# Kernel tuning notes

Hardware: AMD Instinct MI355X
Metric: run time of the kernel (lower is better)

The kernel has to match this reference:

```python
import jax, jax.numpy as jnp
import numpy as np

B, L, D, H = 2, 1024, 1024, 16
HEAD = D // H
BUCKETS = 256
MAX_REL = 512
ATT_SPAN = BUCKETS          # pos_ebd_size = position_buckets when buckets > 0
SCALE_FACTOR = 3            # 1 (content) + 1 (c2p) + 1 (p2c)


def _log_bucket(rel, bucket_size, max_position):
    """make_log_bucket_position: signed log-bucketed relative positions."""
    sign = jnp.sign(rel).astype(jnp.float32)
    mid = bucket_size // 2
    abs_pos = jnp.where((rel < mid) & (rel > -mid), mid - 1, jnp.abs(rel)).astype(jnp.float32)
    log_pos = jnp.ceil(jnp.log(abs_pos / mid) / np.float32(np.log((max_position - 1) / mid)) * (mid - 1)) + mid
    bucket = jnp.where(abs_pos <= mid, rel.astype(jnp.float32), log_pos * sign)
    return bucket.astype(jnp.int32)


def build_relative_position(q_len, k_len):
    rel = jnp.arange(q_len, dtype=jnp.int32)[:, None] - jnp.arange(k_len, dtype=jnp.int32)[None, :]
    return _log_bucket(rel, BUCKETS, MAX_REL)  # [q_len, k_len]


def setup_inputs() -> dict:
    key = jax.random.key(0)
    ks = jax.random.split(key, 6)
    w = 0.02  # typical init scale, keeps softmax well-conditioned
    return {
        "hidden_states": jax.random.normal(ks[0], (B, L, D), jnp.float32),
        "attention_mask": jnp.ones((B, L), jnp.int32),
        "rel_embeddings": jax.random.normal(ks[1], (2 * ATT_SPAN, D), jnp.float32) * w,
        "Wq": jax.random.normal(ks[2], (D, D), jnp.float32) * w,
        "bq": jnp.zeros((D,), jnp.float32),
        "Wk": jax.random.normal(ks[3], (D, D), jnp.float32) * w,
        "bk": jnp.zeros((D,), jnp.float32),
        "Wv": jax.random.normal(ks[4], (D, D), jnp.float32) * w,
        "bv": jnp.zeros((D,), jnp.float32),
    }


def reference(hidden_states, attention_mask, rel_embeddings, Wq, bq, Wk, bk, Wv, bv):
    Bn, Ln, Dn = hidden_states.shape

    def proj(x, W, b):  # Linear with bias, torch convention y = x W^T + b
        return x @ W.T + b

    def to_heads(x):  # [.., L, D] -> [.., H, L, HEAD]
        return x.reshape(*x.shape[:-1], H, HEAD).swapaxes(-3, -2)

    q = to_heads(proj(hidden_states, Wq, bq))  # [B,H,L,d]
    k = to_heads(proj(hidden_states, Wk, bk))
    v = to_heads(proj(hidden_states, Wv, bv))

    scale = jnp.sqrt(jnp.float32(HEAD * SCALE_FACTOR))
    scores = jnp.einsum('bhqd,bhkd->bhqk', q, k) / scale

    # disentangled relative-position bias (share_att_key=True -> reuse Wq/Wk)
    rel = build_relative_position(Ln, Ln)                     # [L,L] log-bucketed
    pos_k = proj(rel_embeddings, Wk, bk).reshape(2 * ATT_SPAN, H, HEAD)
    pos_q = proj(rel_embeddings, Wq, bq).reshape(2 * ATT_SPAN, H, HEAD)

    # c2p: Q . posK, gathered at (rel + span)
    c2p_att = jnp.einsum('bhqd,phd->bhqp', q, pos_k)          # [B,H,L,2S]
    c2p_idx = jnp.clip(rel + ATT_SPAN, 0, 2 * ATT_SPAN - 1)   # [L,L]
    c2p = jnp.take_along_axis(c2p_att, jnp.broadcast_to(c2p_idx[None, None], (Bn, H, Ln, Ln)), axis=-1)

    # p2c: K . posQ gathered at (-rel + span), then transposed to [q,k]
    p2c_att = jnp.einsum('bhkd,phd->bhkp', k, pos_q)          # [B,H,L,2S]
    p2c_idx = jnp.clip(-rel + ATT_SPAN, 0, 2 * ATT_SPAN - 1)
    p2c = jnp.take_along_axis(p2c_att, jnp.broadcast_to(p2c_idx[None, None], (Bn, H, Ln, Ln)), axis=-1)
    p2c = jnp.swapaxes(p2c, -1, -2)

    scores = scores + (c2p + p2c) / scale

    bias = jnp.where(attention_mask[:, None, None, :] > 0, 0.0, -1e9).astype(scores.dtype)
    probs = jax.nn.softmax(scores + bias, axis=-1)
    ctx = jnp.einsum('bhqk,bhkd->bhqd', probs, v)
    return ctx.swapaxes(1, 2).reshape(Bn, Ln, Dn)
```

## Files before the change

### kernel.cpp

```cpp
#include <hip/hip_runtime.h>


typedef short s8v __attribute__((ext_vector_type(8)));
typedef short s4v __attribute__((ext_vector_type(4)));
typedef float f32x4 __attribute__((ext_vector_type(4)));
typedef float f4v __attribute__((ext_vector_type(4)));

#define QK_SCALE 0.26864243f

__device__ __forceinline__ unsigned short f2bf(float f) {
  unsigned u = __builtin_bit_cast(unsigned, f);
  u += 0x7fffu + ((u >> 16) & 1u);
  return (unsigned short)(u >> 16);
}
__device__ __forceinline__ float bf2f(unsigned short h) {
  unsigned u = ((unsigned)h) << 16;
  return __builtin_bit_cast(float, u);
}

__device__ __forceinline__ void gload_lds16(const void* g, void* l) {
  __builtin_amdgcn_global_load_lds(
      (const __attribute__((address_space(1))) void*)g,
      (__attribute__((address_space(3))) void*)l, 16, 0, 0);
}

__global__ __launch_bounds__(256) void prep_kernel(
    const float* __restrict__ hidden, const float* __restrict__ rel,
    const float* __restrict__ Wq, const float* __restrict__ Wk,
    const float* __restrict__ Wv, const int* __restrict__ mask,
    short* __restrict__ Abf, short* __restrict__ Wbf,
    float* __restrict__ mbias, short* __restrict__ Tt) {
  int idx = blockIdx.x * 256 + threadIdx.x;
  const int NCONV = 1441792;
  if (idx < NCONV) {
    const float* src; short* dst; int off;
    if (idx < 524288) { src = hidden; dst = Abf; off = idx; }
    else if (idx < 655360) { src = rel; dst = Abf + 2048 * 1024; off = idx - 524288; }
    else {
      int j = idx - 655360;
      int w = j / 262144; off = j - w * 262144;
      src = (w == 0) ? Wq : (w == 1) ? Wk : Wv;
      dst = Wbf + w * 1048576;
    }
    f4v v = ((const f4v*)src)[off];
    s4v o;
    o[0] = (short)f2bf(v[0]); o[1] = (short)f2bf(v[1]);
    o[2] = (short)f2bf(v[2]); o[3] = (short)f2bf(v[3]);
    ((s4v*)dst)[off] = o;
  } else {
    int j = idx - NCONV;
    if (j < 2047) {
      int r = j - 1023;
      float fr = (float)r;
      float sign = (r > 0) ? 1.f : ((r < 0) ? -1.f : 0.f);
      float abs_pos = (r < 128 && r > -128) ? 127.f : fabsf(fr);
      const float logc = 1.3843393245589053f;
      float log_pos = ceilf(logf(abs_pos * (1.f / 128.f)) / logc * 127.f) + 128.f;
      float bucket = (abs_pos <= 128.f) ? fr : log_pos * sign;
      int bi = (int)bucket + 256;
      bi = bi < 0 ? 0 : (bi > 511 ? 511 : bi);
      Tt[j] = (short)bi;
    } else if (j < 4095) {
      int m = j - 2047;
      mbias[m] = (mask[m] > 0) ? 0.f : -1e9f;
    }
  }
}

__global__ __launch_bounds__(256) void gemm_qkv(
    const short* __restrict__ Abf, const short* __restrict__ Wbf,
    const float* __restrict__ bq, const float* __restrict__ bk,
    const float* __restrict__ bv,
    short* __restrict__ Qc, short* __restrict__ Kc, short* __restrict__ Vc) {
  __shared__ short As[128 * 64];
  __shared__ short Bs[128 * 64];
  int tid = threadIdx.x;
  int wid = tid >> 6, lane = tid & 63;
  int lr = lane & 15, lg = lane >> 4;
  int wr = wid >> 1, wc = wid & 1;
  int z = blockIdx.z;
  int brow = blockIdx.y * 128;
  if (z == 2 && brow >= 2048) return;
  const short* W = Wbf + z * 1048576;
  const float* bias = (z == 0) ? bq : (z == 1) ? bk : bv;
  short* C = (z == 0) ? Qc : (z == 1) ? Kc : Vc;
  float scale = (z == 2) ? 1.f : QK_SCALE;
  int bcol = blockIdx.x * 128;

  f32x4 acc[4][4];
  for (int i = 0; i < 4; i++)
    for (int j = 0; j < 4; j++) acc[i][j] = (f32x4){0.f, 0.f, 0.f, 0.f};

  for (int k0 = 0; k0 < 1024; k0 += 64) {
    for (int i = 0; i < 4; i++) {
      int n = i * 256 + wid * 64 + lane;
      int row = n >> 3, cswz = n & 7, cb = cswz ^ (row & 7);
      const short* gA = Abf + (size_t)(brow + row) * 1024 + k0 + cb * 8;
      gload_lds16(gA, &As[(i * 256 + wid * 64) * 8]);
      const short* gB = W + (size_t)(bcol + row) * 1024 + k0 + cb * 8;
      gload_lds16(gB, &Bs[(i * 256 + wid * 64) * 8]);
    }
    __syncthreads();
    for (int ks = 0; ks < 2; ks++) {
      s8v af[4], bfv[4];
      for (int mi = 0; mi < 4; mi++) {
        int row = wr * 64 + mi * 16 + lr, cb = ks * 4 + lg;
        af[mi] = *(const s8v*)&As[row * 64 + (cb ^ (row & 7)) * 8];
      }
      for (int ni = 0; ni < 4; ni++) {
        int row = wc * 64 + ni * 16 + lr, cb = ks * 4 + lg;
        bfv[ni] = *(const s8v*)&Bs[row * 64 + (cb ^ (row & 7)) * 8];
      }
      for (int mi = 0; mi < 4; mi++)
        for (int ni = 0; ni < 4; ni++)
          acc[mi][ni] = __builtin_amdgcn_mfma_f32_16x16x32_bf16(
              af[mi], bfv[ni], acc[mi][ni], 0, 0, 0);
    }
    __syncthreads();
  }
  for (int mi = 0; mi < 4; mi++)
    for (int ni = 0; ni < 4; ni++) {
      int col = bcol + wc * 64 + ni * 16 + lr;
      float bb = bias[col];
      for (int r = 0; r < 4; r++) {
        int row = brow + wr * 64 + mi * 16 + lg * 4 + r;
        float v = (acc[mi][ni][r] + bb) * scale;
        C[(size_t)row * 1024 + col] = (short)f2bf(v);
      }
    }
}

__global__ __launch_bounds__(256) void pos_trans(
    const short* __restrict__ Qc, const short* __restrict__ Kc,
    const short* __restrict__ Vc, const float* __restrict__ mbias,
    short* __restrict__ c2p, short* __restrict__ p2c,
    short* __restrict__ Vt) {
  __shared__ short sh[2 * 128 * 64];
  int tid = threadIdx.x;
  if (blockIdx.z < 64) {
    short* As = sh;
    short* Bs = sh + 128 * 64;
    int wid = tid >> 6, lane = tid & 63;
    int lr = lane & 15, lg = lane >> 4;
    int wr = wid >> 1, wc = wid & 1;
    int zz = blockIdx.z;
    int which = zz >> 5;
    int bh = zz & 31;
    int b = bh >> 4, h = bh & 15;
    const short* Arows = (which == 0) ? Qc : Kc;
    const short* Brows = (which == 0) ? Kc : Qc;
    short* Out = (which == 0) ? c2p : p2c;
    int mrow = blockIdx.y * 128;
    int ncol = blockIdx.x * 128;

    for (int i = 0; i < 4; i++) {
      int n = i * 256 + wid * 64 + lane;
      int row = n >> 3, cswz = n & 7, cb = cswz ^ (row & 7);
      const short* gA = Arows + (size_t)(b * 1024 + mrow + row) * 1024 + h * 64 + cb * 8;
      gload_lds16(gA, &As[(i * 256 + wid * 64) * 8]);
      const short* gB = Brows + (size_t)(2048 + ncol + row) * 1024 + h * 64 + cb * 8;
      gload_lds16(gB, &Bs[(i * 256 + wid * 64) * 8]);
    }
    __syncthreads();

    f32x4 acc[4][4];
    for (int i = 0; i < 4; i++)
      for (int j = 0; j < 4; j++) acc[i][j] = (f32x4){0.f, 0.f, 0.f, 0.f};
    for (int ks = 0; ks < 2; ks++) {
      s8v af[4], bfv[4];
      for (int mi = 0; mi < 4; mi++) {
        int row = wr * 64 + mi * 16 + lr, cb = ks * 4 + lg;
        af[mi] = *(const s8v*)&As[row * 64 + (cb ^ (row & 7)) * 8];
      }
      for (int ni = 0; ni < 4; ni++) {
        int row = wc * 64 + ni * 16 + lr, cb = ks * 4 + lg;
        bfv[ni] = *(const s8v*)&Bs[row * 64 + (cb ^ (row & 7)) * 8];
      }
      for (int mi = 0; mi < 4; mi++)
        for (int ni = 0; ni < 4; ni++)
          acc[mi][ni] = __builtin_amdgcn_mfma_f32_16x16x32_bf16(
              af[mi], bfv[ni], acc[mi][ni], 0, 0, 0);
    }
    size_t base = (size_t)(b * 16 + h) * 1024;
    for (int mi = 0; mi < 4; mi++)
      for (int ni = 0; ni < 4; ni++)
        for (int r = 0; r < 4; r++) {
          int m = mrow + wr * 64 + mi * 16 + lg * 4 + r;
          int nn = ncol + wc * 64 + ni * 16 + lr;
          float v = acc[mi][ni][r];
          if (which == 1) v += mbias[b * 1024 + m];
          Out[(base + m) * 512 + nn] = (short)f2bf(v);
        }
  } else {
    short* TL = sh;
    int idx = ((blockIdx.z - 64) * 8 + blockIdx.y) * 4 + blockIdx.x;
    int b = idx >> 8, h = (idx >> 4) & 15, lt = idx & 15;
    for (int i = 0; i < 2; i++) {
      int n = i * 256 + tid;
      int l = n >> 3, c = n & 7;
      s8v v = *(const s8v*)&Vc[(size_t)(b * 1024 + lt * 64 + l) * 1024 + h * 64 + c * 8];
      *(s8v*)&TL[l * 72 + c * 8] = v;
    }
    __syncthreads();
    for (int i = 0; i < 2; i++) {
      int m = i * 256 + tid;
      int d = m >> 3, c = m & 7;
      s8v o;
      for (int jj = 0; jj < 8; jj++) o[jj] = TL[(c * 8 + jj) * 72 + d];
      *(s8v*)&Vt[((size_t)(b * 16 + h) * 64 + d) * 1024 + lt * 64 + c * 8] = o;
    }
  }
}

__global__ __launch_bounds__(256) void bias_build(
    const short* __restrict__ c2p, const short* __restrict__ p2c,
    const short* __restrict__ Tt, short* __restrict__ bias) {
  __shared__ short Wc[64 * 66];
  __shared__ short Wp[64 * 66];
  __shared__ short Tl[128];
  int tid = threadIdx.x;
  int wid = tid >> 6, lane = tid & 63;
  int lr = lane & 15, lg = lane >> 4;
  int qt = blockIdx.x, kt = blockIdx.y, bh = blockIdx.z;
  int q0 = qt * 64, k0 = kt * 64;
  int relbase = q0 - k0;
  size_t bh1024 = (size_t)bh * 1024;

  if (tid < 127) Tl[tid] = Tt[relbase + 960 + tid];
  __syncthreads();

#pragma unroll
  for (int ii = 0; ii < 16; ii++) {
    int row = wid * 16 + ii;
    int w0 = Tl[row];
    int col = w0 + lane; col = col > 511 ? 511 : col;
    Wc[row * 66 + lane] = c2p[(bh1024 + q0 + row) * 512 + col];
    int w0p_ = Tl[63 - row];
    int colp = w0p_ + lane; colp = colp > 511 ? 511 : colp;
    Wp[row * 66 + lane] = p2c[(bh1024 + k0 + row) * 512 + colp];
  }
  __syncthreads();

  int w0c[4], w0p[4];
#pragma unroll
  for (int r = 0; r < 4; r++) w0c[r] = Tl[wid * 16 + lg * 4 + r];
#pragma unroll
  for (int n = 0; n < 4; n++) w0p[n] = Tl[63 - (n * 16 + lr)];

  s8v o0, o1;
#pragma unroll
  for (int n = 0; n < 4; n++)
#pragma unroll
    for (int r = 0; r < 4; r++) {
      int qq = wid * 16 + lg * 4 + r;
      int kk = n * 16 + lr;
      int p = Tl[qq - kk + 63];
      float v = bf2f((unsigned short)Wc[qq * 66 + p - w0c[r]]) +
                bf2f((unsigned short)Wp[kk * 66 + p - w0p[n]]);
      short s = (short)f2bf(v);
      if (n < 2) o0[(n & 1) * 4 + r] = s; else o1[(n & 1) * 4 + r] = s;
    }
  size_t tile = ((size_t)bh * 16 + qt) * 16 + kt;
  size_t base = (tile * 4 + wid) * 1024 + lane * 8;
  *(s8v*)&bias[base] = o0;
  *(s8v*)&bias[base + 512] = o1;
}

template <int NSPLIT>
__global__ __launch_bounds__(256) void attn_frag(
    const short* __restrict__ Qc, const short* __restrict__ Kc,
    const short* __restrict__ Vt, const short* __restrict__ bias,
    float* __restrict__ Opart, float* __restrict__ dpart,
    float* __restrict__ out) {
  const int KSEG = 1024 / NSPLIT;
  const int NT = KSEG / 64;
  __shared__ short Kl[2][64 * 64];
  __shared__ short Vl[2][64 * 64];
  __shared__ short Pl[4][16 * 64];
  int tid = threadIdx.x;
  int wid = tid >> 6, lane = tid & 63;
  int lr = lane & 15, lg = lane >> 4;
  int qt = blockIdx.x, h = blockIdx.y, z = blockIdx.z;
  int b = (NSPLIT == 1) ? z : (z / NSPLIT);
  int ks = (NSPLIT == 1) ? 0 : (z % NSPLIT);
  int k0seg = ks * KSEG;
  int q0 = qt * 64, qbase = q0 + wid * 16;

  s8v aq[2];
  for (int s_ = 0; s_ < 2; s_++)
    aq[s_] = *(const s8v*)&Qc[(size_t)(b * 1024 + qbase + lr) * 1024 + h * 64 + s_ * 32 + lg * 8];

  f32x4 oacc[4];
  for (int n = 0; n < 4; n++) oacc[n] = (f32x4){0.f, 0.f, 0.f, 0.f};
  float dsum[4] = {0.f, 0.f, 0.f, 0.f};

  auto stage = [&](int t, int buf) {
#pragma unroll
    for (int i = 0; i < 2; i++) {
      int n = i * 256 + tid;
      int row = n >> 3, cswz = n & 7, cb = cswz ^ (row & 7);
      gload_lds16(&Kc[(size_t)(b * 1024 + k0seg + t * 64 + row) * 1024 + h * 64 + cb * 8],
                  &Kl[buf][(i * 256 + wid * 64) * 8]);
      gload_lds16(&Vt[((size_t)(b * 16 + h) * 64 + row) * 1024 + k0seg + t * 64 + cb * 8],
                  &Vl[buf][(i * 256 + wid * 64) * 8]);
    }
  };
  auto fload = [&](int t, s8v& f0, s8v& f1) {
    size_t tile = (((size_t)(b * 16 + h) * 16 + qt) * 16 + (k0seg >> 6) + t);
    size_t base = (tile * 4 + wid) * 1024 + lane * 8;
    f0 = *(const s8v*)&bias[base];
    f1 = *(const s8v*)&bias[base + 512];
  };

  s8v fb0, fb1, fn0, fn1;
  stage(0, 0);
  fload(0, fb0, fb1);
  __syncthreads();

#pragma unroll
  for (int t = 0; t < NT; ++t) {
    const int cur = t & 1, nxt = cur ^ 1;

    if (t + 1 < NT) {
      stage(t + 1, nxt);
      fload(t + 1, fn0, fn1);
    }

    f32x4 sacc[4];
#pragma unroll
    for (int n = 0; n < 4; n++) sacc[n] = (f32x4){0.f, 0.f, 0.f, 0.f};
#pragma unroll
    for (int s_ = 0; s_ < 2; s_++)
#pragma unroll
      for (int n = 0; n < 4; n++) {
        int row = n * 16 + lr, cb = s_ * 4 + lg, cbs = cb ^ (row & 7);
        s8v bk_ = *(const s8v*)&Kl[cur][row * 64 + cbs * 8];
        sacc[n] = __builtin_amdgcn_mfma_f32_16x16x32_bf16(aq[s_], bk_, sacc[n], 0, 0, 0);
      }

#pragma unroll
    for (int n = 0; n < 4; n++)
#pragma unroll
      for (int r = 0; r < 4; r++) {
        unsigned short bv_ = (unsigned short)((n < 2 ? fb0 : fb1)[(n & 1) * 4 + r]);
        float p = __expf(sacc[n][r] + bf2f(bv_));
        dsum[r] += p;
        int prow = lg * 4 + r, pc = n * 16 + lr;
        int pcb = (pc >> 3) ^ (prow & 7);
        Pl[wid][prow * 64 + pcb * 8 + (pc & 7)] = (short)f2bf(p);
      }
    asm volatile("s_waitcnt lgkmcnt(0)" ::: "memory");

#pragma unroll
    for (int s_ = 0; s_ < 2; s_++) {
      int pcb = (s_ * 4 + lg) ^ (lr & 7);
      s8v ap = *(const s8v*)&Pl[wid][lr * 64 + pcb * 8];
#pragma unroll
      for (int n = 0; n < 4; n++) {
        int row = n * 16 + lr, cb = s_ * 4 + lg, cbs = cb ^ (row & 7);
        s8v bv_ = *(const s8v*)&Vl[cur][row * 64 + cbs * 8];
        oacc[n] = __builtin_amdgcn_mfma_f32_16x16x32_bf16(ap, bv_, oacc[n], 0, 0, 0);
      }
    }

    __syncthreads();

    if (t + 1 < NT) { fb0 = fn0; fb1 = fn1; }
  }

  for (int m = 1; m < 16; m <<= 1)
    for (int r = 0; r < 4; r++) dsum[r] += __shfl_xor(dsum[r], m, 64);

  if (NSPLIT == 1) {
    for (int n = 0; n < 4; n++)
      for (int r = 0; r < 4; r++) {
        int q = qbase + lg * 4 + r;
        int d = n * 16 + lr;
        out[(size_t)(b * 1024 + q) * 1024 + h * 64 + d] = oacc[n][r] / dsum[r];
      }
  } else {
    size_t po = ((size_t)(z * 16 + h)) * 65536;
    for (int n = 0; n < 4; n++)
      for (int r = 0; r < 4; r++) {
        int q = qbase + lg * 4 + r;
        Opart[po + (size_t)q * 64 + n * 16 + lr] = oacc[n][r];
      }
    if (lr == 0)
      for (int r = 0; r < 4; r++)
        dpart[(z * 16 + h) * 1024 + qbase + lg * 4 + r] = dsum[r];
  }
}

template <int NSPLIT>
__global__ __launch_bounds__(256) void attn_gather(
    const short* __restrict__ Qc, const short* __restrict__ Kc,
    const short* __restrict__ Vt, const short* __restrict__ c2p,
    const short* __restrict__ p2c, const short* __restrict__ Tt,
    float* __restrict__ Opart, float* __restrict__ dpart,
    float* __restrict__ out) {
  const int KSEG = 1024 / NSPLIT;
  const int NT = KSEG / 64;
  const int TLN = 64 + KSEG - 1;
  __shared__ short Kl[2][64 * 64];
  __shared__ short Vl[2][64 * 64];
  __shared__ short Pl[4][16 * 72];
  __shared__ short Tl[TLN + 1];
  int tid = threadIdx.x;
  int wid = tid >> 6, lane = tid & 63;
  int lr = lane & 15, lg = lane >> 4;
  int qt = blockIdx.x, h = blockIdx.y, z = blockIdx.z;
  int b = (NSPLIT == 1) ? z : (z / NSPLIT);
  int ks = (NSPLIT == 1) ? 0 : (z % NSPLIT);
  int k0seg = ks * KSEG;
  int q0 = qt * 64, qbase = q0 + wid * 16;
  size_t bh1024 = (size_t)(b * 16 + h) * 1024;

  for (int i = tid; i < TLN; i += 256) Tl[i] = Tt[(q0 - k0seg - (KSEG - 1) + 1023) + i];

  s8v aq[2];
  for (int s_ = 0; s_ < 2; s_++)
    aq[s_] = *(const s8v*)&Qc[(size_t)(b * 1024 + qbase + lr) * 1024 + h * 64 + s_ * 32 + lg * 8];

  f32x4 oacc[4];
  for (int n = 0; n < 4; n++) oacc[n] = (f32x4){0.f, 0.f, 0.f, 0.f};
  float dsum[4] = {0.f, 0.f, 0.f, 0.f};
  __syncthreads();

  auto stage = [&](int t, int buf) {
#pragma unroll
    for (int i = 0; i < 2; i++) {
      int n = i * 256 + tid;
      int row = n >> 3, cswz = n & 7, cb = cswz ^ (row & 7);
      gload_lds16(&Kc[(size_t)(b * 1024 + k0seg + t * 64 + row) * 1024 + h * 64 + cb * 8],
                  &Kl[buf][(i * 256 + wid * 64) * 8]);
      gload_lds16(&Vt[((size_t)(b * 16 + h) * 64 + row) * 1024 + k0seg + t * 64 + cb * 8],
                  &Vl[buf][(i * 256 + wid * 64) * 8]);
    }
  };
  auto gather = [&](int t, unsigned short* cg, unsigned short* pg) {
#pragma unroll
    for (int n = 0; n < 4; n++) {
      int k = k0seg + t * 64 + n * 16 + lr;
      size_t prow = (bh1024 + k) * 512;
      int jb = wid * 16 - t * 64 - lr + (KSEG - 1) - n * 16 + lg * 4;
#pragma unroll
      for (int r = 0; r < 4; r++) {
        int q = qbase + lg * 4 + r;
        int idx = Tl[jb + r];
        cg[n * 4 + r] = (unsigned short)c2p[(bh1024 + q) * 512 + idx];
        pg[n * 4 + r] = (unsigned short)p2c[prow + idx];
      }
    }
  };

  unsigned short c2g[16], p2g[16], c2n[16], p2n[16];
  stage(0, 0);
  gather(0, c2g, p2g);
  __syncthreads();

#pragma unroll
  for (int t = 0; t < NT; ++t) {
    const int cur = t & 1, nxt = cur ^ 1;
    if (t + 1 < NT) { stage(t + 1, nxt); gather(t + 1, c2n, p2n); }

    f32x4 sacc[4];
#pragma unroll
    for (int n = 0; n < 4; n++) sacc[n] = (f32x4){0.f, 0.f, 0.f, 0.f};
#pragma unroll
    for (int s_ = 0; s_ < 2; s_++)
#pragma unroll
      for (int n = 0; n < 4; n++) {
        int row = n * 16 + lr, cb = s_ * 4 + lg, cbs = cb ^ (row & 7);
        s8v bk_ = *(const s8v*)&Kl[cur][row * 64 + cbs * 8];
        sacc[n] = __builtin_amdgcn_mfma_f32_16x16x32_bf16(aq[s_], bk_, sacc[n], 0, 0, 0);
      }
#pragma unroll
    for (int n = 0; n < 4; n++)
#pragma unroll
      for (int r = 0; r < 4; r++) {
        float bias = bf2f(c2g[n * 4 + r]) + bf2f(p2g[n * 4 + r]);
        float p = __expf(sacc[n][r] + bias);
        dsum[r] += p;
        Pl[wid][(lg * 4 + r) * 72 + n * 16 + lr] = (short)f2bf(p);
      }
    asm volatile("s_waitcnt lgkmcnt(0)" ::: "memory");
#pragma unroll
    for (int s_ = 0; s_ < 2; s_++) {
      s8v ap = *(const s8v*)&Pl[wid][lr * 72 + s_ * 32 + lg * 8];
#pragma unroll
      for (int n = 0; n < 4; n++) {
        int row = n * 16 + lr, cb = s_ * 4 + lg, cbs = cb ^ (row & 7);
        s8v bv_ = *(const s8v*)&Vl[cur][row * 64 + cbs * 8];
        oacc[n] = __builtin_amdgcn_mfma_f32_16x16x32_bf16(ap, bv_, oacc[n], 0, 0, 0);
      }
    }
    __syncthreads();
    if (t + 1 < NT) {
#pragma unroll
      for (int i = 0; i < 16; i++) { c2g[i] = c2n[i]; p2g[i] = p2n[i]; }
    }
  }

  for (int m = 1; m < 16; m <<= 1)
    for (int r = 0; r < 4; r++) dsum[r] += __shfl_xor(dsum[r], m, 64);

  if (NSPLIT == 1) {
    for (int n = 0; n < 4; n++)
      for (int r = 0; r < 4; r++) {
        int q = qbase + lg * 4 + r;
        int d = n * 16 + lr;
        out[(size_t)(b * 1024 + q) * 1024 + h * 64 + d] = oacc[n][r] / dsum[r];
      }
  } else {
    size_t po = ((size_t)(z * 16 + h)) * 65536;
    for (int n = 0; n < 4; n++)
      for (int r = 0; r < 4; r++) {
        int q = qbase + lg * 4 + r;
        Opart[po + (size_t)q * 64 + n * 16 + lr] = oacc[n][r];
      }
    if (lr == 0)
      for (int r = 0; r < 4; r++)
        dpart[(z * 16 + h) * 1024 + qbase + lg * 4 + r] = dsum[r];
  }
}

template <int NSPLIT>
__global__ __launch_bounds__(256) void combine_kernel(
    const float* __restrict__ Opart, const float* __restrict__ dpart,
    float* __restrict__ out) {
  int idx = blockIdx.x * 256 + threadIdx.x;
  int pos = idx * 4;
  int b = pos >> 20;
  int q = (pos >> 10) & 1023;
  int hd = pos & 1023;
  int h = hd >> 6, d = hd & 63;
  f4v s = (f4v){0.f, 0.f, 0.f, 0.f};
  float dn = 0.f;
  for (int ks = 0; ks < NSPLIT; ks++) {
    int zh = (b * NSPLIT + ks) * 16 + h;
    s += *(const f4v*)&Opart[(size_t)zh * 65536 + q * 64 + d];
    dn += dpart[zh * 1024 + q];
  }
  f4v r = s / dn;
  *(f4v*)&out[pos] = r;
}

extern "C" void kernel_launch(void* const* d_in, const int* in_sizes, int n_in,
                              void* d_out, int out_size, void* d_ws, size_t ws_size,
                              hipStream_t stream) {
  (void)in_sizes; (void)n_in; (void)out_size;
  const float* hidden = (const float*)d_in[0];
  const int* mask = (const int*)d_in[1];
  const float* rel = (const float*)d_in[2];
  const float* Wq = (const float*)d_in[3];
  const float* bq = (const float*)d_in[4];
  const float* Wk = (const float*)d_in[5];
  const float* bk = (const float*)d_in[6];
  const float* Wv = (const float*)d_in[7];
  const float* bv = (const float*)d_in[8];
  float* out = (float*)d_out;

  char* w = (char*)d_ws;
  short* Abf = (short*)w; w += 2560 * 1024 * 2;
  short* Wbf = (short*)w; w += 3 * 1024 * 1024 * 2;
  short* Qc  = (short*)w; w += 2560 * 1024 * 2;
  short* Kc  = (short*)w; w += 2560 * 1024 * 2;
  short* Vc  = (short*)w; w += 2560 * 1024 * 2;
  short* Vt  = (short*)w; w += 2 * 16 * 64 * 1024 * 2;
  short* c2p = (short*)w; w += (size_t)2 * 16 * 1024 * 512 * 2;
  short* p2c = (short*)w; w += (size_t)2 * 16 * 1024 * 512 * 2;
  short* Tt  = (short*)w; w += 4096;
  float* mbias = (float*)w; w += 8192;
  short* bias_frag = (short*)w;
  size_t need_frag = (size_t)(w - (char*)d_ws) + (size_t)8192 * 4096 * 2;
  float* Opart_old = (float*)w;
  size_t need_old = (size_t)(w - (char*)d_ws) + (size_t)8 * 16 * 1024 * 64 * 4 + 8 * 16 * 1024 * 4;

  prep_kernel<<<5648, 256, 0, stream>>>(hidden, rel, Wq, Wk, Wv, mask, Abf, Wbf, mbias, Tt);
  gemm_qkv<<<dim3(8, 20, 3), 256, 0, stream>>>(Abf, Wbf, bq, bk, bv, Qc, Kc, Vc);
  pos_trans<<<dim3(4, 8, 80), 256, 0, stream>>>(Qc, Kc, Vc, mbias, c2p, p2c, Vt);

  if (ws_size >= need_frag) {
    float* Opart = (float*)c2p;
    float* dpart = (float*)p2c;
    bias_build<<<dim3(16, 16, 32), 256, 0, stream>>>(c2p, p2c, Tt, bias_frag);
    attn_frag<2><<<dim3(16, 16, 4), 256, 0, stream>>>(Qc, Kc, Vt, bias_frag,
                                                      Opart, dpart, out);
    combine_kernel<2><<<2048, 256, 0, stream>>>(Opart, dpart, out);
  } else if (ws_size >= need_old) {
    float* Opart = Opart_old;
    float* dpart = (float*)((char*)Opart_old + (size_t)8 * 16 * 1024 * 64 * 4);
    attn_gather<4><<<dim3(16, 16, 8), 256, 0, stream>>>(Qc, Kc, Vt, c2p, p2c, Tt,
                                                        Opart, dpart, out);
    combine_kernel<4><<<2048, 256, 0, stream>>>(Opart, dpart, out);
  } else {
    attn_gather<1><<<dim3(16, 16, 2), 256, 0, stream>>>(Qc, Kc, Vt, c2p, p2c, Tt,
                                                        (float*)Opart_old, (float*)Opart_old, out);
  }
}
```

Before: 136.5 us.

## Split key range across waves within block and reduce in LDS, dropping combine kernel

Replaces the global split-K attention (NSPLIT=2 across grid plus a separate combine kernel) with a 32-query-row block where two wave pairs each process half of the key tiles, then reduce partial outputs and denominators through shared memory before writing the normalized result. This removes the partial-output global writes/reads and the extra combine launch. In exchange, every block still stages all 16 K/V tiles while each wave computes on only half, so half the waves idle per iteration and LDS loading per useful work doubles.

```diff
diff --git a/kernel.cpp b/kernel.cpp
--- a/kernel.cpp
+++ b/kernel.cpp
@@ -266,25 +266,21 @@
   *(s8v*)&bias[base + 512] = o1;
 }
 
-template <int NSPLIT>
-__global__ __launch_bounds__(256) void attn_frag(
+__global__ __launch_bounds__(256) void attn_frag32(
     const short* __restrict__ Qc, const short* __restrict__ Kc,
     const short* __restrict__ Vt, const short* __restrict__ bias,
-    float* __restrict__ Opart, float* __restrict__ dpart,
     float* __restrict__ out) {
-  const int KSEG = 1024 / NSPLIT;
-  const int NT = KSEG / 64;
   __shared__ short Kl[2][64 * 64];
   __shared__ short Vl[2][64 * 64];
   __shared__ short Pl[4][16 * 64];
   int tid = threadIdx.x;
   int wid = tid >> 6, lane = tid & 63;
   int lr = lane & 15, lg = lane >> 4;
-  int qt = blockIdx.x, h = blockIdx.y, z = blockIdx.z;
-  int b = (NSPLIT == 1) ? z : (z / NSPLIT);
-  int ks = (NSPLIT == 1) ? 0 : (z % NSPLIT);
-  int k0seg = ks * KSEG;
-  int q0 = qt * 64, qbase = q0 + wid * 16;
+  int qt = blockIdx.x, h = blockIdx.y, b = blockIdx.z;
+  int qsub = wid & 1, khalf = wid >> 1;
+  int qbase = qt * 32 + qsub * 16;
+  int quarter = (qt & 1) * 2 + qsub;
+  size_t bh16 = (size_t)(b * 16 + h);
 
   s8v aq[2];
   for (int s_ = 0; s_ < 2; s_++)
@@ -299,95 +295,99 @@
     for (int i = 0; i < 2; i++) {
       int n = i * 256 + tid;
       int row = n >> 3, cswz = n & 7, cb = cswz ^ (row & 7);
-      gload_lds16(&Kc[(size_t)(b * 1024 + k0seg + t * 64 + row) * 1024 + h * 64 + cb * 8],
+      gload_lds16(&Kc[(size_t)(b * 1024 + t * 64 + row) * 1024 + h * 64 + cb * 8],
                   &Kl[buf][(i * 256 + wid * 64) * 8]);
-      gload_lds16(&Vt[((size_t)(b * 16 + h) * 64 + row) * 1024 + k0seg + t * 64 + cb * 8],
+      gload_lds16(&Vt[(bh16 * 64 + row) * 1024 + t * 64 + cb * 8],
                   &Vl[buf][(i * 256 + wid * 64) * 8]);
     }
   };
   auto fload = [&](int t, s8v& f0, s8v& f1) {
-    size_t tile = (((size_t)(b * 16 + h) * 16 + qt) * 16 + (k0seg >> 6) + t);
-    size_t base = (tile * 4 + wid) * 1024 + lane * 8;
+    size_t tile = (bh16 * 16 + (qt >> 1)) * 16 + t;
+    size_t base = (tile * 4 + quarter) * 1024 + lane * 8;
     f0 = *(const s8v*)&bias[base];
     f1 = *(const s8v*)&bias[base + 512];
   };
 
   s8v fb0, fb1, fn0, fn1;
   stage(0, 0);
-  fload(0, fb0, fb1);
+  if (khalf == 0) fload(0, fb0, fb1);
   __syncthreads();
 
 #pragma unroll
-  for (int t = 0; t < NT; ++t) {
+  for (int t = 0; t < 16; ++t) {
     const int cur = t & 1, nxt = cur ^ 1;
-
-    if (t + 1 < NT) {
+    const bool active = ((t >> 3) == khalf);
+
+    if (t + 1 < 16) {
       stage(t + 1, nxt);
-      fload(t + 1, fn0, fn1);
-    }
-
-    f32x4 sacc[4];
-#pragma unroll
-    for (int n = 0; n < 4; n++) sacc[n] = (f32x4){0.f, 0.f, 0.f, 0.f};
-#pragma unroll
-    for (int s_ = 0; s_ < 2; s_++)
-#pragma unroll
-      for (int n = 0; n < 4; n++) {
-        int row = n * 16 + lr, cb = s_ * 4 + lg, cbs = cb ^ (row & 7);
-        s8v bk_ = *(const s8v*)&Kl[cur][row * 64 + cbs * 8];
-        sacc[n] = __builtin_amdgcn_mfma_f32_16x16x32_bf16(aq[s_], bk_, sacc[n], 0, 0, 0);
-      }
-
-#pragma unroll
-    for (int n = 0; n < 4; n++)
-#pragma unroll
-      for (int r = 0; r < 4; r++) {
-        unsigned short bv_ = (unsigned short)((n < 2 ? fb0 : fb1)[(n & 1) * 4 + r]);
-        float p = __expf(sacc[n][r] + bf2f(bv_));
-        dsum[r] += p;
-        int prow = lg * 4 + r, pc = n * 16 + lr;
-        int pcb = (pc >> 3) ^ (prow & 7);
-        Pl[wid][prow * 64 + pcb * 8 + (pc & 7)] = (short)f2bf(p);
-      }
-    asm volatile("s_waitcnt lgkmcnt(0)" ::: "memory");
-
-#pragma unroll
-    for (int s_ = 0; s_ < 2; s_++) {
-      int pcb = (s_ * 4 + lg) ^ (lr & 7);
-      s8v ap = *(const s8v*)&Pl[wid][lr * 64 + pcb * 8];
-#pragma unroll
-      for (int n = 0; n < 4; n++) {
-        int row = n * 16 + lr, cb = s_ * 4 + lg, cbs = cb ^ (row & 7);
-        s8v bv_ = *(const s8v*)&Vl[cur][row * 64 + cbs * 8];
-        oacc[n] = __builtin_amdgcn_mfma_f32_16x16x32_bf16(ap, bv_, oacc[n], 0, 0, 0);
+      if (((t + 1) >> 3) == khalf) fload(t + 1, fn0, fn1);
+    }
+
+    if (active) {
+      f32x4 sacc[4];
+#pragma unroll
+      for (int n = 0; n < 4; n++) sacc[n] = (f32x4){0.f, 0.f, 0.f, 0.f};
+#pragma unroll
+      for (int s_ = 0; s_ < 2; s_++)
+#pragma unroll
+        for (int n = 0; n < 4; n++) {
+          int row = n * 16 + lr, cb = s_ * 4 + lg, cbs = cb ^ (row & 7);
+          s8v bk_ = *(const s8v*)&Kl[cur][row * 64 + cbs * 8];
+          sacc[n] = __builtin_amdgcn_mfma_f32_16x16x32_bf16(aq[s_], bk_, sacc[n], 0, 0, 0);
+        }
+
+#pragma unroll
+      for (int n = 0; n < 4; n++)
+#pragma unroll
+        for (int r = 0; r < 4; r++) {
+          unsigned short bv_ = (unsigned short)((n < 2 ? fb0 : fb1)[(n & 1) * 4 + r]);
+          float p = __expf(sacc[n][r] + bf2f(bv_));
+          dsum[r] += p;
+          int prow = lg * 4 + r, pc = n * 16 + lr;
+          int pcb = (pc >> 3) ^ (prow & 7);
+          Pl[wid][prow * 64 + pcb * 8 + (pc & 7)] = (short)f2bf(p);
+        }
+      asm volatile("s_waitcnt lgkmcnt(0)" ::: "memory");
+
+#pragma unroll
+      for (int s_ = 0; s_ < 2; s_++) {
+        int pcb = (s_ * 4 + lg) ^ (lr & 7);
+        s8v ap = *(const s8v*)&Pl[wid][lr * 64 + pcb * 8];
+#pragma unroll
+        for (int n = 0; n < 4; n++) {
+          int row = n * 16 + lr, cb = s_ * 4 + lg, cbs = cb ^ (row & 7);
+          s8v bv_ = *(const s8v*)&Vl[cur][row * 64 + cbs * 8];
+          oacc[n] = __builtin_amdgcn_mfma_f32_16x16x32_bf16(ap, bv_, oacc[n], 0, 0, 0);
+        }
       }
     }
 
     __syncthreads();
 
-    if (t + 1 < NT) { fb0 = fn0; fb1 = fn1; }
+    fb0 = fn0; fb1 = fn1;
   }
 
   for (int m = 1; m < 16; m <<= 1)
     for (int r = 0; r < 4; r++) dsum[r] += __shfl_xor(dsum[r], m, 64);
 
-  if (NSPLIT == 1) {
+  float* Ol = (float*)&Kl[0][0];
+  float* Dl = (float*)&Pl[0][0];
+  for (int n = 0; n < 4; n++)
+    for (int r = 0; r < 4; r++)
+      Ol[wid * 1024 + (lg * 4 + r) * 64 + n * 16 + lr] = oacc[n][r];
+  if (lr == 0)
+    for (int r = 0; r < 4; r++) Dl[wid * 16 + lg * 4 + r] = dsum[r];
+  __syncthreads();
+  if (khalf == 0) {
+    int pw = wid + 2;
+    float dtot[4];
+    for (int r = 0; r < 4; r++) dtot[r] = dsum[r] + Dl[pw * 16 + lg * 4 + r];
     for (int n = 0; n < 4; n++)
       for (int r = 0; r < 4; r++) {
+        float o = oacc[n][r] + Ol[pw * 1024 + (lg * 4 + r) * 64 + n * 16 + lr];
         int q = qbase + lg * 4 + r;
-        int d = n * 16 + lr;
-        out[(size_t)(b * 1024 + q) * 1024 + h * 64 + d] = oacc[n][r] / dsum[r];
-      }
-  } else {
-    size_t po = ((size_t)(z * 16 + h)) * 65536;
-    for (int n = 0; n < 4; n++)
-      for (int r = 0; r < 4; r++) {
-        int q = qbase + lg * 4 + r;
-        Opart[po + (size_t)q * 64 + n * 16 + lr] = oacc[n][r];
-      }
-    if (lr == 0)
-      for (int r = 0; r < 4; r++)
-        dpart[(z * 16 + h) * 1024 + qbase + lg * 4 + r] = dsum[r];
+        out[(size_t)(b * 1024 + q) * 1024 + h * 64 + n * 16 + lr] = o / dtot[r];
+      }
   }
 }
 
@@ -581,12 +581,8 @@
   pos_trans<<<dim3(4, 8, 80), 256, 0, stream>>>(Qc, Kc, Vc, mbias, c2p, p2c, Vt);
 
   if (ws_size >= need_frag) {
-    float* Opart = (float*)c2p;
-    float* dpart = (float*)p2c;
     bias_build<<<dim3(16, 16, 32), 256, 0, stream>>>(c2p, p2c, Tt, bias_frag);
-    attn_frag<2><<<dim3(16, 16, 4), 256, 0, stream>>>(Qc, Kc, Vt, bias_frag,
-                                                      Opart, dpart, out);
-    combine_kernel<2><<<2048, 256, 0, stream>>>(Opart, dpart, out);
+    attn_frag32<<<dim3(32, 16, 2), 256, 0, stream>>>(Qc, Kc, Vt, bias_frag, out);
   } else if (ws_size >= need_old) {
     float* Opart = Opart_old;
     float* dpart = (float*)((char*)Opart_old + (size_t)8 * 16 * 1024 * 64 * 4);
```

Measured after the change: 135.0 us. About the same (-1.1%).
